# Kernel optimization log

Hardware: AMD Instinct MI355X
Metric: run time of the kernel (lower is better)

Reference implementation:

```python
import jax, jax.numpy as jnp
import numpy as np

N = 100000   # nodes
E = 625000   # edges
D = 128      # feature / embedding dim
C = 40       # num classes
BN_EPS = 1e-5
L2_EPS = 1e-12


def setup_inputs() -> dict:
    key = jax.random.key(0)
    ks = jax.random.split(key, 8)
    s = 1.0 / np.sqrt(D)
    return {
        "x": jax.random.normal(ks[0], (N, D), dtype=jnp.float32),
        "edge_index": jax.random.randint(ks[1], (2, E), 0, N, dtype=jnp.int64),
        "W1": jax.random.normal(ks[2], (D, D), dtype=jnp.float32) * s,
        "b1": jnp.zeros((D,), jnp.float32),
        "W2": jax.random.normal(ks[3], (D, D), dtype=jnp.float32) * s,
        "b2": jnp.zeros((D,), jnp.float32),
        "W3": jax.random.normal(ks[4], (D, D), dtype=jnp.float32) * s,
        "b3": jnp.zeros((D,), jnp.float32),
        "g1": jnp.ones((D,), jnp.float32), "be1": jnp.zeros((D,), jnp.float32),
        "g2": jnp.ones((D,), jnp.float32), "be2": jnp.zeros((D,), jnp.float32),
        "g3": jnp.ones((D,), jnp.float32), "be3": jnp.zeros((D,), jnp.float32),
        "Wout": jax.random.normal(ks[5], (D, C), dtype=jnp.float32) * s,
        "bout": jnp.zeros((C,), jnp.float32),
    }


def _gcn_norm(edge_index, n):
    # PyG GCNConv default: add self loops, symmetric normalization
    loop = jnp.arange(n)
    src = jnp.concatenate([edge_index[0], loop])
    dst = jnp.concatenate([edge_index[1], loop])
    deg = jax.ops.segment_sum(jnp.ones_like(src, dtype=jnp.float32), dst, num_segments=n)
    dinv = jnp.where(deg > 0, jax.lax.rsqrt(deg), 0.0)
    norm = dinv[src] * dinv[dst]  # [E+N]
    return src, dst, norm


def _gcn_conv(x, W, b, src, dst, norm, n):
    h = x @ W                                # [N, D]
    msg = h[src] * norm[:, None]             # gather, [E+N, D]
    out = jax.ops.segment_sum(msg, dst, num_segments=n)  # scatter-add
    return out + b


def _bn(x, g, b):
    mu = jnp.mean(x, axis=0)
    var = jnp.var(x, axis=0)
    return (x - mu) * jax.lax.rsqrt(var + BN_EPS) * g + b


def _l2norm(x):
    n = jnp.sqrt(jnp.sum(x * x, axis=1, keepdims=True))
    return x / jnp.maximum(n, L2_EPS)


def reference(x, edge_index, W1, b1, W2, b2, W3, b3,
              g1, be1, g2, be2, g3, be3, Wout, bout):
    n = x.shape[0]
    src, dst, norm = _gcn_norm(edge_index, n)

    h = jax.nn.relu(_bn(_gcn_conv(x, W1, b1, src, dst, norm, n), g1, be1))
    h = _l2norm(h)
    r = h
    h = jax.nn.relu(_bn(_gcn_conv(h, W2, b2, src, dst, norm, n), g2, be2))
    h = _l2norm(h + r)
    r = h
    h = jax.nn.relu(_bn(_gcn_conv(h, W3, b3, src, dst, norm, n), g3, be3))
    h = _l2norm(h + r)

    return h @ Wout + bout  # node classification logits [N, C]
```

## Files before the change

### kernel.cpp

```cpp
#include <hip/hip_runtime.h>
#include <math.h>

#define DD 128
#define COUT 40
#define BN_EPS 1e-5f
#define L2_EPS 1e-12f

typedef __attribute__((ext_vector_type(8))) short bf16x8;
typedef __attribute__((ext_vector_type(4))) float f32x4;

static __device__ inline unsigned short f2bf(float f) {
    unsigned int x = __float_as_uint(f);
    unsigned int r = (x + 0x7FFFu + ((x >> 16) & 1u)) >> 16;
    return (unsigned short)r;
}
static __device__ inline float bf2f(unsigned short u) {
    return __uint_as_float(((unsigned int)u) << 16);
}


__global__ void k_init(int* deg, int* fill, int n) {
    int i = blockIdx.x * blockDim.x + threadIdx.x;
    if (i < n) { deg[i] = 1; fill[i] = 0; }
}

__global__ void k_hist(const int* ei, int E, int* deg) {
    int i = blockIdx.x * blockDim.x + threadIdx.x;
    if (i < E) atomicAdd(&deg[ei[E + i]], 1);
}

__global__ void k_dinv(const int* deg, float* dinv, int n) {
    int i = blockIdx.x * blockDim.x + threadIdx.x;
    if (i < n) dinv[i] = rsqrtf((float)deg[i]);
}

__global__ void k_scan_a(const int* deg, int* row_ptr, int* bsum, int n) {
    __shared__ int s[256];
    int t = threadIdx.x;
    int idx = blockIdx.x * 256 + t;
    int v = (idx < n) ? deg[idx] : 0;
    s[t] = v; __syncthreads();
    for (int off = 1; off < 256; off <<= 1) {
        int x = (t >= off) ? s[t - off] : 0;
        __syncthreads(); s[t] += x; __syncthreads();
    }
    if (idx <= n) row_ptr[idx] = s[t] - v;
    if (t == 255) bsum[blockIdx.x] = s[255];
}

__global__ void k_scan_b(const int* bsum, int* boff, int nb) {
    __shared__ int s[512];
    int t = threadIdx.x;
    int v = (t < nb) ? bsum[t] : 0;
    s[t] = v; __syncthreads();
    for (int off = 1; off < 512; off <<= 1) {
        int x = (t >= off) ? s[t - off] : 0;
        __syncthreads(); s[t] += x; __syncthreads();
    }
    if (t < nb) boff[t] = s[t] - v;
}

__global__ void k_scan_c(int* row_ptr, const int* boff, int n1) {
    int idx = blockIdx.x * blockDim.x + threadIdx.x;
    if (idx < n1) row_ptr[idx] += boff[idx >> 8];
}

__global__ void k_fill(const int* ei, int E, int n, const int* row_ptr,
                       const float* dinv, int* fill, int2* epair) {
    int i = blockIdx.x * blockDim.x + threadIdx.x;
    int total = E + n;
    if (i >= total) return;
    int u, v;
    if (i < E) { u = ei[i]; v = ei[E + i]; }
    else { u = i - E; v = u; }
    int p = atomicAdd(&fill[v], 1);
    int pos = row_ptr[v] + p;
    int2 pr; pr.x = u; pr.y = __float_as_int(dinv[u]);
    epair[pos] = pr;
}

__global__ void k_wrepack_all(const float* __restrict__ W1, const float* __restrict__ W2,
                              const float* __restrict__ W3, const float* __restrict__ Wout,
                              unsigned short* __restrict__ wb,
                              unsigned short* __restrict__ wob,
                              float* __restrict__ stats) {
    int b = blockIdx.x;
    if (b < 24) {
        int wi = b >> 3;
        const float* W = (wi == 0) ? W1 : (wi == 1) ? W2 : W3;
        unsigned short* out = wb + wi * 16384;
        int idx = (b & 7) * 256 + threadIdx.x;
        int kc = idx >> 9;
        int cc = (idx >> 6) & 7;
        int lane = idx & 63;
        int n = cc * 16 + (lane & 15);
        int kb = kc * 32 + (lane >> 4) * 8;
        unsigned short tmp[8];
#pragma unroll
        for (int j = 0; j < 8; j++) tmp[j] = f2bf(W[(size_t)(kb + j) * DD + n]);
        *(uint4*)&out[(size_t)idx * 8] = *(const uint4*)tmp;
    } else if (b < 27) {
        int idx = (b - 24) * 256 + threadIdx.x;
        int kc = idx / 192;
        int rem = idx % 192;
        int cc = rem >> 6;
        int lane = rem & 63;
        int n = cc * 16 + (lane & 15);
        int kb = kc * 32 + (lane >> 4) * 8;
        unsigned short tmp[8];
#pragma unroll
        for (int j = 0; j < 8; j++)
            tmp[j] = (n < COUT) ? f2bf(Wout[(size_t)(kb + j) * COUT + n]) : 0;
        *(uint4*)&wob[(size_t)idx * 8] = *(const uint4*)tmp;
    } else {
        stats[threadIdx.x] = 0.f;
        stats[256 + threadIdx.x] = 0.f;
        stats[512 + threadIdx.x] = 0.f;
    }
}


__global__ __launch_bounds__(256) void k_gemm0(const float* __restrict__ A,
                                               const unsigned short* __restrict__ Wb,
                                               unsigned short* __restrict__ C, int nrows) {
    __shared__ __align__(16) unsigned short Ws[16384];
    const int tid = threadIdx.x;
    for (int i = tid; i < 2048; i += 256)
        ((uint4*)Ws)[i] = ((const uint4*)Wb)[i];
    __syncthreads();

    const int wv = tid >> 6;
    const int lane = tid & 63;
    const int R0 = blockIdx.x * 64 + wv * 16;
    if (R0 >= nrows) return;
    const int m = lane & 15, q = lane >> 4;
    int rr = R0 + m; if (rr >= nrows) rr = nrows - 1;
    const float* Ar = A + (size_t)rr * DD + q * 8;

    bf16x8 af[4];
#pragma unroll
    for (int kc = 0; kc < 4; kc++) {
        float4 lo = *(const float4*)(Ar + kc * 32);
        float4 hi = *(const float4*)(Ar + kc * 32 + 4);
        unsigned short t[8];
        t[0] = f2bf(lo.x); t[1] = f2bf(lo.y); t[2] = f2bf(lo.z); t[3] = f2bf(lo.w);
        t[4] = f2bf(hi.x); t[5] = f2bf(hi.y); t[6] = f2bf(hi.z); t[7] = f2bf(hi.w);
        af[kc] = *(const bf16x8*)t;
    }

    f32x4 acc[8];
#pragma unroll
    for (int cc = 0; cc < 8; cc++) acc[cc] = (f32x4){0.f, 0.f, 0.f, 0.f};
#pragma unroll
    for (int kc = 0; kc < 4; kc++)
#pragma unroll
        for (int cc = 0; cc < 8; cc++) {
            bf16x8 b = *(const bf16x8*)&Ws[(size_t)((kc * 8 + cc) * 64 + lane) * 8];
            acc[cc] = __builtin_amdgcn_mfma_f32_16x16x32_bf16(af[kc], b, acc[cc], 0, 0, 0);
        }

#pragma unroll
    for (int cc = 0; cc < 8; cc++)
#pragma unroll
        for (int i = 0; i < 4; i++) {
            int r = R0 + q * 4 + i;
            if (r < nrows) C[(size_t)r * DD + cc * 16 + m] = f2bf(acc[cc][i]);
        }
}

__global__ void k_agg(const unsigned short* __restrict__ lin, const int* __restrict__ row_ptr,
                      const int2* __restrict__ epair, const float* __restrict__ dinv,
                      const float* __restrict__ bias, unsigned short* __restrict__ outb, int n) {
    int lane = threadIdx.x;
    int half = lane >> 5;
    int li = lane & 31;
    int v = blockIdx.x * 8 + threadIdx.y * 2 + half;
    if (v >= n) return;
    int c = li * 4;
    int s = row_ptr[v], e = row_ptr[v + 1];
    float dv = dinv[v];
    float4 accA = *(const float4*)&bias[c];
    float4 accB = make_float4(0.f, 0.f, 0.f, 0.f);
    int j = s;
    for (; j + 1 < e; j += 2) {
        int2 p0 = epair[j], p1 = epair[j + 1];
        float w0 = dv * __int_as_float(p0.y);
        float w1 = dv * __int_as_float(p1.y);
        ushort4 t0 = *(const ushort4*)&lin[(size_t)p0.x * DD + c];
        ushort4 t1 = *(const ushort4*)&lin[(size_t)p1.x * DD + c];
        accA.x += w0 * bf2f(t0.x); accA.y += w0 * bf2f(t0.y);
        accA.z += w0 * bf2f(t0.z); accA.w += w0 * bf2f(t0.w);
        accB.x += w1 * bf2f(t1.x); accB.y += w1 * bf2f(t1.y);
        accB.z += w1 * bf2f(t1.z); accB.w += w1 * bf2f(t1.w);
    }
    if (j < e) {
        int2 p = epair[j];
        float w = dv * __int_as_float(p.y);
        ushort4 t = *(const ushort4*)&lin[(size_t)p.x * DD + c];
        accA.x += w * bf2f(t.x); accA.y += w * bf2f(t.y);
        accA.z += w * bf2f(t.z); accA.w += w * bf2f(t.w);
    }
    accA.x += accB.x; accA.y += accB.y; accA.z += accB.z; accA.w += accB.w;
    ushort4 o;
    o.x = f2bf(accA.x); o.y = f2bf(accA.y); o.z = f2bf(accA.z); o.w = f2bf(accA.w);
    *(ushort4*)&outb[(size_t)v * DD + c] = o;
}

__global__ __launch_bounds__(256) void k_bnstats(const unsigned short* __restrict__ X, int n,
                                                 float* __restrict__ stats) {
    int cg = (threadIdx.x & 31) * 4;
    int rg = threadIdx.x >> 5;
    float s0 = 0, s1 = 0, s2 = 0, s3 = 0;
    float q0 = 0, q1 = 0, q2 = 0, q3 = 0;
    for (int r = blockIdx.x * 8 + rg; r < n; r += gridDim.x * 8) {
        ushort4 xv = *(const ushort4*)&X[(size_t)r * DD + cg];
        float x0 = bf2f(xv.x), x1 = bf2f(xv.y), x2 = bf2f(xv.z), x3 = bf2f(xv.w);
        s0 += x0; s1 += x1; s2 += x2; s3 += x3;
        q0 += x0 * x0; q1 += x1 * x1; q2 += x2 * x2; q3 += x3 * x3;
    }
    __shared__ float sh[8][128];
    __shared__ float qh[8][128];
    sh[rg][cg] = s0; sh[rg][cg + 1] = s1; sh[rg][cg + 2] = s2; sh[rg][cg + 3] = s3;
    qh[rg][cg] = q0; qh[rg][cg + 1] = q1; qh[rg][cg + 2] = q2; qh[rg][cg + 3] = q3;
    __syncthreads();
    if (threadIdx.x < 128) {
        float a = 0, b = 0;
        for (int g = 0; g < 8; g++) { a += sh[g][threadIdx.x]; b += qh[g][threadIdx.x]; }
        atomicAdd(&stats[threadIdx.x], a);
        atomicAdd(&stats[128 + threadIdx.x], b);
    }
}

template <bool HAS_RES>
__global__ __launch_bounds__(256) void k_fused(const unsigned short* __restrict__ aggX,
                                               const float* __restrict__ stats,
                                               const float* __restrict__ g,
                                               const float* __restrict__ be, float inv_n,
                                               const unsigned short* __restrict__ resb,
                                               const unsigned short* __restrict__ Wb,
                                               unsigned short* __restrict__ hbf_out,
                                               unsigned short* __restrict__ linb_out,
                                               int nrows) {
    __shared__ __align__(16) unsigned short Ws[16384];
    __shared__ float ssl[256];
    const int tid = threadIdx.x;
    for (int i = tid; i < 2048; i += 256)
        ((uint4*)Ws)[i] = ((const uint4*)Wb)[i];
    if (tid < 128) {
        float mu = stats[tid] * inv_n;
        float var = stats[128 + tid] * inv_n - mu * mu;
        float sc = g[tid] * rsqrtf(var + BN_EPS);
        ssl[tid] = sc;
        ssl[128 + tid] = be[tid] - mu * sc;
    }
    __syncthreads();

    const int wv = tid >> 6;
    const int lane = tid & 63;
    const int R0 = blockIdx.x * 64 + wv * 16;
    if (R0 >= nrows) return;
    const int m = lane & 15, q = lane >> 4;
    int rr = R0 + m; if (rr >= nrows) rr = nrows - 1;
    const unsigned short* Ar = aggX + (size_t)rr * DD + q * 8;
    const unsigned short* Rr = HAS_RES ? resb + (size_t)rr * DD + q * 8 : nullptr;

    float y[4][8];
    float sq = 0.f;
#pragma unroll
    for (int kc = 0; kc < 4; kc++) {
        ushort4 lo = *(const ushort4*)(Ar + kc * 32);
        ushort4 hi = *(const ushort4*)(Ar + kc * 32 + 4);
        unsigned short av[8] = {lo.x, lo.y, lo.z, lo.w, hi.x, hi.y, hi.z, hi.w};
        int c0 = kc * 32 + q * 8;
        float4 sc0 = *(const float4*)&ssl[c0];
        float4 sc1 = *(const float4*)&ssl[c0 + 4];
        float4 sh0 = *(const float4*)&ssl[128 + c0];
        float4 sh1 = *(const float4*)&ssl[128 + c0 + 4];
        float scv[8] = {sc0.x, sc0.y, sc0.z, sc0.w, sc1.x, sc1.y, sc1.z, sc1.w};
        float shv[8] = {sh0.x, sh0.y, sh0.z, sh0.w, sh1.x, sh1.y, sh1.z, sh1.w};
        if (HAS_RES) {
            ushort4 rl = *(const ushort4*)(Rr + kc * 32);
            ushort4 rh = *(const ushort4*)(Rr + kc * 32 + 4);
            unsigned short rv[8] = {rl.x, rl.y, rl.z, rl.w, rh.x, rh.y, rh.z, rh.w};
#pragma unroll
            for (int j = 0; j < 8; j++) {
                float yy = fmaxf(bf2f(av[j]) * scv[j] + shv[j], 0.f) + bf2f(rv[j]);
                y[kc][j] = yy; sq += yy * yy;
            }
        } else {
#pragma unroll
            for (int j = 0; j < 8; j++) {
                float yy = fmaxf(bf2f(av[j]) * scv[j] + shv[j], 0.f);
                y[kc][j] = yy; sq += yy * yy;
            }
        }
    }
    sq += __shfl_xor(sq, 16, 64);
    sq += __shfl_xor(sq, 32, 64);
    float inv = 1.f / fmaxf(sqrtf(sq), L2_EPS);

    bf16x8 af[4];
#pragma unroll
    for (int kc = 0; kc < 4; kc++) {
        unsigned short t[8];
#pragma unroll
        for (int j = 0; j < 8; j++) t[j] = f2bf(y[kc][j] * inv);
        af[kc] = *(const bf16x8*)t;
        *(bf16x8*)&hbf_out[(size_t)rr * DD + q * 8 + kc * 32] = af[kc];
    }

    f32x4 acc[8];
#pragma unroll
    for (int cc = 0; cc < 8; cc++) acc[cc] = (f32x4){0.f, 0.f, 0.f, 0.f};
#pragma unroll
    for (int kc = 0; kc < 4; kc++)
#pragma unroll
        for (int cc = 0; cc < 8; cc++) {
            bf16x8 b = *(const bf16x8*)&Ws[(size_t)((kc * 8 + cc) * 64 + lane) * 8];
            acc[cc] = __builtin_amdgcn_mfma_f32_16x16x32_bf16(af[kc], b, acc[cc], 0, 0, 0);
        }

#pragma unroll
    for (int cc = 0; cc < 8; cc++)
#pragma unroll
        for (int i = 0; i < 4; i++) {
            int r = R0 + q * 4 + i;
            if (r < nrows) linb_out[(size_t)r * DD + cc * 16 + m] = f2bf(acc[cc][i]);
        }
}

__global__ __launch_bounds__(256) void k_outfused(const unsigned short* __restrict__ aggX,
                                                  const float* __restrict__ stats,
                                                  const float* __restrict__ g,
                                                  const float* __restrict__ be, float inv_n,
                                                  const unsigned short* __restrict__ resb,
                                                  const unsigned short* __restrict__ wob,
                                                  const float* __restrict__ bout,
                                                  float* __restrict__ C, int nrows) {
    __shared__ __align__(16) unsigned short Ws[6144];
    __shared__ float ssl[256];
    const int tid = threadIdx.x;
    for (int i = tid; i < 768; i += 256)
        ((uint4*)Ws)[i] = ((const uint4*)wob)[i];
    if (tid < 128) {
        float mu = stats[tid] * inv_n;
        float var = stats[128 + tid] * inv_n - mu * mu;
        float sc = g[tid] * rsqrtf(var + BN_EPS);
        ssl[tid] = sc;
        ssl[128 + tid] = be[tid] - mu * sc;
    }
    __syncthreads();

    const int wv = tid >> 6;
    const int lane = tid & 63;
    const int R0 = blockIdx.x * 64 + wv * 16;
    if (R0 >= nrows) return;
    const int m = lane & 15, q = lane >> 4;
    int rr = R0 + m; if (rr >= nrows) rr = nrows - 1;
    const unsigned short* Ar = aggX + (size_t)rr * DD + q * 8;
    const unsigned short* Rr = resb + (size_t)rr * DD + q * 8;

    float y[4][8];
    float sq = 0.f;
#pragma unroll
    for (int kc = 0; kc < 4; kc++) {
        ushort4 lo = *(const ushort4*)(Ar + kc * 32);
        ushort4 hi = *(const ushort4*)(Ar + kc * 32 + 4);
        ushort4 rl = *(const ushort4*)(Rr + kc * 32);
        ushort4 rh = *(const ushort4*)(Rr + kc * 32 + 4);
        unsigned short av[8] = {lo.x, lo.y, lo.z, lo.w, hi.x, hi.y, hi.z, hi.w};
        unsigned short rv[8] = {rl.x, rl.y, rl.z, rl.w, rh.x, rh.y, rh.z, rh.w};
        int c0 = kc * 32 + q * 8;
        float4 sc0 = *(const float4*)&ssl[c0];
        float4 sc1 = *(const float4*)&ssl[c0 + 4];
        float4 sh0 = *(const float4*)&ssl[128 + c0];
        float4 sh1 = *(const float4*)&ssl[128 + c0 + 4];
        float scv[8] = {sc0.x, sc0.y, sc0.z, sc0.w, sc1.x, sc1.y, sc1.z, sc1.w};
        float shv[8] = {sh0.x, sh0.y, sh0.z, sh0.w, sh1.x, sh1.y, sh1.z, sh1.w};
#pragma unroll
        for (int j = 0; j < 8; j++) {
            float yy = fmaxf(bf2f(av[j]) * scv[j] + shv[j], 0.f) + bf2f(rv[j]);
            y[kc][j] = yy; sq += yy * yy;
        }
    }
    sq += __shfl_xor(sq, 16, 64);
    sq += __shfl_xor(sq, 32, 64);
    float inv = 1.f / fmaxf(sqrtf(sq), L2_EPS);

    bf16x8 af[4];
#pragma unroll
    for (int kc = 0; kc < 4; kc++) {
        unsigned short t[8];
#pragma unroll
        for (int j = 0; j < 8; j++) t[j] = f2bf(y[kc][j] * inv);
        af[kc] = *(const bf16x8*)t;
    }

    f32x4 acc[3];
#pragma unroll
    for (int cc = 0; cc < 3; cc++) acc[cc] = (f32x4){0.f, 0.f, 0.f, 0.f};
#pragma unroll
    for (int kc = 0; kc < 4; kc++)
#pragma unroll
        for (int cc = 0; cc < 3; cc++) {
            bf16x8 b = *(const bf16x8*)&Ws[(size_t)((kc * 3 + cc) * 64 + lane) * 8];
            acc[cc] = __builtin_amdgcn_mfma_f32_16x16x32_bf16(af[kc], b, acc[cc], 0, 0, 0);
        }

#pragma unroll
    for (int cc = 0; cc < 3; cc++) {
        int col = cc * 16 + m;
        if (col < COUT) {
            float bb = bout[col];
#pragma unroll
            for (int i = 0; i < 4; i++) {
                int r = R0 + q * 4 + i;
                if (r < nrows) C[(size_t)r * COUT + col] = acc[cc][i] + bb;
            }
        }
    }
}


extern "C" void kernel_launch(void* const* d_in, const int* in_sizes, int n_in,
                              void* d_out, int out_size, void* d_ws, size_t ws_size,
                              hipStream_t stream) {
    const float* x    = (const float*)d_in[0];
    const int*   ei   = (const int*)d_in[1];
    const float* W1   = (const float*)d_in[2];
    const float* b1   = (const float*)d_in[3];
    const float* W2   = (const float*)d_in[4];
    const float* b2   = (const float*)d_in[5];
    const float* W3   = (const float*)d_in[6];
    const float* b3   = (const float*)d_in[7];
    const float* g1   = (const float*)d_in[8];
    const float* be1  = (const float*)d_in[9];
    const float* g2   = (const float*)d_in[10];
    const float* be2  = (const float*)d_in[11];
    const float* g3   = (const float*)d_in[12];
    const float* be3  = (const float*)d_in[13];
    const float* Wout = (const float*)d_in[14];
    const float* bout = (const float*)d_in[15];
    float* out = (float*)d_out;

    const int N = in_sizes[0] / DD;
    const int E = in_sizes[1] / 2;
    const int NNZ = E + N;

    char* w = (char*)d_ws;
    unsigned short* linb = (unsigned short*)w; w += (size_t)N * DD * sizeof(unsigned short);
    unsigned short* aggA = (unsigned short*)w; w += (size_t)N * DD * sizeof(unsigned short);
    unsigned short* aggB = (unsigned short*)w; w += (size_t)N * DD * sizeof(unsigned short);
    unsigned short* hbf1 = (unsigned short*)w; w += (size_t)N * DD * sizeof(unsigned short);
    unsigned short* hbf2 = (unsigned short*)w; w += (size_t)N * DD * sizeof(unsigned short);
    unsigned short* wb   = (unsigned short*)w; w += 3 * 16384 * sizeof(unsigned short);
    unsigned short* wob  = (unsigned short*)w; w += 6144 * sizeof(unsigned short);
    int2* epair  = (int2*)w;                   w += (size_t)NNZ * sizeof(int2);
    int* deg     = (int*)w;                    w += (size_t)N * sizeof(int);
    int* fill    = (int*)w;                    w += (size_t)N * sizeof(int);
    int* row_ptr = (int*)w;                    w += (size_t)(N + 1) * sizeof(int);
    float* dinv  = (float*)w;                  w += (size_t)N * sizeof(float);
    int* bsum    = (int*)w;                    w += 512 * sizeof(int);
    int* boff    = (int*)w;                    w += 512 * sizeof(int);
    float* stats = (float*)w;                  w += 768 * sizeof(float);

    const int NB = (N + 1 + 255) / 256;
    const int STATS_GRID = 128;

    k_init<<<(N + 255) / 256, 256, 0, stream>>>(deg, fill, N);
    k_hist<<<(E + 255) / 256, 256, 0, stream>>>(ei, E, deg);
    k_dinv<<<(N + 255) / 256, 256, 0, stream>>>(deg, dinv, N);
    k_scan_a<<<NB, 256, 0, stream>>>(deg, row_ptr, bsum, N);
    k_scan_b<<<1, 512, 0, stream>>>(bsum, boff, NB);
    k_scan_c<<<(N + 1 + 255) / 256, 256, 0, stream>>>(row_ptr, boff, N + 1);
    k_fill<<<(NNZ + 255) / 256, 256, 0, stream>>>(ei, E, N, row_ptr, dinv, fill, epair);
    k_wrepack_all<<<28, 256, 0, stream>>>(W1, W2, W3, Wout, wb, wob, stats);

    int gemmGrid = (N + 63) / 64;
    dim3 aggGrid((N + 7) / 8);
    dim3 aggBlk(64, 4);
    float inv_n = 1.0f / (float)N;

    k_gemm0<<<gemmGrid, 256, 0, stream>>>(x, wb, linb, N);
    k_agg<<<aggGrid, aggBlk, 0, stream>>>(linb, row_ptr, epair, dinv, b1, aggA, N);
    k_bnstats<<<STATS_GRID, 256, 0, stream>>>(aggA, N, stats);
    k_fused<false><<<gemmGrid, 256, 0, stream>>>(aggA, stats, g1, be1, inv_n,
                                                 nullptr, wb + 16384, hbf1, linb, N);
    k_agg<<<aggGrid, aggBlk, 0, stream>>>(linb, row_ptr, epair, dinv, b2, aggB, N);
    k_bnstats<<<STATS_GRID, 256, 0, stream>>>(aggB, N, stats + 256);
    k_fused<true><<<gemmGrid, 256, 0, stream>>>(aggB, stats + 256, g2, be2, inv_n,
                                                hbf1, wb + 32768, hbf2, linb, N);
    k_agg<<<aggGrid, aggBlk, 0, stream>>>(linb, row_ptr, epair, dinv, b3, aggA, N);
    k_bnstats<<<STATS_GRID, 256, 0, stream>>>(aggA, N, stats + 512);
    k_outfused<<<gemmGrid, 256, 0, stream>>>(aggA, stats + 512, g3, be3, inv_n,
                                             hbf2, wob, bout, out, N);
}
```

Baseline: 474.1 us.

## Fuse BN statistics into aggregation and simplify CSR build with recorded atomic positions

Aggregation is rewritten so one wavefront handles one node. Four lane groups each take a different edge and load 8 bf16 channels, then combine partial sums with cross-lane shuffles. The same kernel accumulates the BatchNorm sum and sum of squares, which removes the separate stats pass that reread the aggregated features. CSR construction records each edge's atomic slot during the histogram, folds the dinv computation into the scan, places self-loops at the end of each row, and replaces the init kernel with a memset. Together these cut four launches, the fill atomics and one full feature reread per layer. The cost is a persistent grid of 2048 blocks that does more shuffle work, and the order of edges inside each row changes.

```diff
diff --git a/kernel.cpp b/kernel.cpp
--- a/kernel.cpp
+++ b/kernel.cpp
@@ -19,26 +19,19 @@
 }
 
 
-__global__ void k_init(int* deg, int* fill, int n) {
+__global__ void k_hist(const int* __restrict__ ei, int E, int* __restrict__ deg,
+                       int* __restrict__ pord) {
     int i = blockIdx.x * blockDim.x + threadIdx.x;
-    if (i < n) { deg[i] = 1; fill[i] = 0; }
-}
-
-__global__ void k_hist(const int* ei, int E, int* deg) {
-    int i = blockIdx.x * blockDim.x + threadIdx.x;
-    if (i < E) atomicAdd(&deg[ei[E + i]], 1);
-}
-
-__global__ void k_dinv(const int* deg, float* dinv, int n) {
-    int i = blockIdx.x * blockDim.x + threadIdx.x;
-    if (i < n) dinv[i] = rsqrtf((float)deg[i]);
-}
-
-__global__ void k_scan_a(const int* deg, int* row_ptr, int* bsum, int n) {
+    if (i < E) pord[i] = atomicAdd(&deg[ei[E + i]], 1);
+}
+
+__global__ void k_scan_a(const int* __restrict__ deg, int* __restrict__ row_ptr,
+                         int* __restrict__ bsum, float* __restrict__ dinv, int n) {
     __shared__ int s[256];
     int t = threadIdx.x;
     int idx = blockIdx.x * 256 + t;
-    int v = (idx < n) ? deg[idx] : 0;
+    int v = (idx < n) ? deg[idx] + 1 : 0;
+    if (idx < n) dinv[idx] = rsqrtf((float)v);
     s[t] = v; __syncthreads();
     for (int off = 1; off < 256; off <<= 1) {
         int x = (t >= off) ? s[t - off] : 0;
@@ -48,7 +41,7 @@
     if (t == 255) bsum[blockIdx.x] = s[255];
 }
 
-__global__ void k_scan_b(const int* bsum, int* boff, int nb) {
+__global__ void k_scan_b(const int* __restrict__ bsum, int* __restrict__ boff, int nb) {
     __shared__ int s[512];
     int t = threadIdx.x;
     int v = (t < nb) ? bsum[t] : 0;
@@ -60,21 +53,26 @@
     if (t < nb) boff[t] = s[t] - v;
 }
 
-__global__ void k_scan_c(int* row_ptr, const int* boff, int n1) {
+__global__ void k_scan_c(int* __restrict__ row_ptr, const int* __restrict__ boff, int n1) {
     int idx = blockIdx.x * blockDim.x + threadIdx.x;
     if (idx < n1) row_ptr[idx] += boff[idx >> 8];
 }
 
-__global__ void k_fill(const int* ei, int E, int n, const int* row_ptr,
-                       const float* dinv, int* fill, int2* epair) {
+__global__ void k_fill(const int* __restrict__ ei, const int* __restrict__ pord,
+                       int E, int n, const int* __restrict__ row_ptr,
+                       const float* __restrict__ dinv, int2* __restrict__ epair) {
     int i = blockIdx.x * blockDim.x + threadIdx.x;
     int total = E + n;
     if (i >= total) return;
-    int u, v;
-    if (i < E) { u = ei[i]; v = ei[E + i]; }
-    else { u = i - E; v = u; }
-    int p = atomicAdd(&fill[v], 1);
-    int pos = row_ptr[v] + p;
+    int u, pos;
+    if (i < E) {
+        u = ei[i];
+        int v = ei[E + i];
+        pos = row_ptr[v] + pord[i];
+    } else {
+        u = i - E;
+        pos = row_ptr[u + 1] - 1;
+    }
     int2 pr; pr.x = u; pr.y = __float_as_int(dinv[u]);
     epair[pos] = pr;
 }
@@ -168,66 +166,102 @@
         }
 }
 
-__global__ void k_agg(const unsigned short* __restrict__ lin, const int* __restrict__ row_ptr,
-                      const int2* __restrict__ epair, const float* __restrict__ dinv,
-                      const float* __restrict__ bias, unsigned short* __restrict__ outb, int n) {
-    int lane = threadIdx.x;
-    int half = lane >> 5;
-    int li = lane & 31;
-    int v = blockIdx.x * 8 + threadIdx.y * 2 + half;
-    if (v >= n) return;
-    int c = li * 4;
-    int s = row_ptr[v], e = row_ptr[v + 1];
-    float dv = dinv[v];
-    float4 accA = *(const float4*)&bias[c];
-    float4 accB = make_float4(0.f, 0.f, 0.f, 0.f);
-    int j = s;
-    for (; j + 1 < e; j += 2) {
-        int2 p0 = epair[j], p1 = epair[j + 1];
-        float w0 = dv * __int_as_float(p0.y);
-        float w1 = dv * __int_as_float(p1.y);
-        ushort4 t0 = *(const ushort4*)&lin[(size_t)p0.x * DD + c];
-        ushort4 t1 = *(const ushort4*)&lin[(size_t)p1.x * DD + c];
-        accA.x += w0 * bf2f(t0.x); accA.y += w0 * bf2f(t0.y);
-        accA.z += w0 * bf2f(t0.z); accA.w += w0 * bf2f(t0.w);
-        accB.x += w1 * bf2f(t1.x); accB.y += w1 * bf2f(t1.y);
-        accB.z += w1 * bf2f(t1.z); accB.w += w1 * bf2f(t1.w);
-    }
-    if (j < e) {
-        int2 p = epair[j];
-        float w = dv * __int_as_float(p.y);
-        ushort4 t = *(const ushort4*)&lin[(size_t)p.x * DD + c];
-        accA.x += w * bf2f(t.x); accA.y += w * bf2f(t.y);
-        accA.z += w * bf2f(t.z); accA.w += w * bf2f(t.w);
-    }
-    accA.x += accB.x; accA.y += accB.y; accA.z += accB.z; accA.w += accB.w;
-    ushort4 o;
-    o.x = f2bf(accA.x); o.y = f2bf(accA.y); o.z = f2bf(accA.z); o.w = f2bf(accA.w);
-    *(ushort4*)&outb[(size_t)v * DD + c] = o;
-}
-
-__global__ __launch_bounds__(256) void k_bnstats(const unsigned short* __restrict__ X, int n,
-                                                 float* __restrict__ stats) {
-    int cg = (threadIdx.x & 31) * 4;
-    int rg = threadIdx.x >> 5;
-    float s0 = 0, s1 = 0, s2 = 0, s3 = 0;
-    float q0 = 0, q1 = 0, q2 = 0, q3 = 0;
-    for (int r = blockIdx.x * 8 + rg; r < n; r += gridDim.x * 8) {
-        ushort4 xv = *(const ushort4*)&X[(size_t)r * DD + cg];
-        float x0 = bf2f(xv.x), x1 = bf2f(xv.y), x2 = bf2f(xv.z), x3 = bf2f(xv.w);
-        s0 += x0; s1 += x1; s2 += x2; s3 += x3;
-        q0 += x0 * x0; q1 += x1 * x1; q2 += x2 * x2; q3 += x3 * x3;
-    }
-    __shared__ float sh[8][128];
-    __shared__ float qh[8][128];
-    sh[rg][cg] = s0; sh[rg][cg + 1] = s1; sh[rg][cg + 2] = s2; sh[rg][cg + 3] = s3;
-    qh[rg][cg] = q0; qh[rg][cg + 1] = q1; qh[rg][cg + 2] = q2; qh[rg][cg + 3] = q3;
+__global__ __launch_bounds__(256) void k_aggs(const unsigned short* __restrict__ lin,
+                                              const int* __restrict__ row_ptr,
+                                              const int2* __restrict__ epair,
+                                              const float* __restrict__ dinv,
+                                              const float* __restrict__ bias,
+                                              unsigned short* __restrict__ outb,
+                                              float* __restrict__ stats, int n) {
+    const int tid = threadIdx.x;
+    const int wv = tid >> 6;
+    const int lane = tid & 63;
+    const int g = lane >> 4;
+    const int ci = (lane & 15) * 8;
+
+    float bs[8];
+    {
+        float4 b0 = *(const float4*)&bias[ci];
+        float4 b1 = *(const float4*)&bias[ci + 4];
+        bs[0] = b0.x; bs[1] = b0.y; bs[2] = b0.z; bs[3] = b0.w;
+        bs[4] = b1.x; bs[5] = b1.y; bs[6] = b1.z; bs[7] = b1.w;
+    }
+
+    float s[8], q[8];
+#pragma unroll
+    for (int k = 0; k < 8; k++) { s[k] = 0.f; q[k] = 0.f; }
+
+    const int wstride = gridDim.x * 4;
+    for (int v = blockIdx.x * 4 + wv; v < n; v += wstride) {
+        int rp0 = row_ptr[v];
+        int deg = row_ptr[v + 1] - rp0;
+        float dv = dinv[v];
+        float acc[8];
+#pragma unroll
+        for (int k = 0; k < 8; k++) acc[k] = 0.f;
+
+        for (int j = 0; j < deg; j += 8) {
+            int i0 = j + g;
+            int i1 = j + 4 + g;
+            if (i0 < deg) {
+                int2 p = epair[rp0 + i0];
+                float w = dv * __int_as_float(p.y);
+                uint4 t = *(const uint4*)&lin[(size_t)p.x * DD + ci];
+                acc[0] += w * __uint_as_float(t.x << 16);
+                acc[1] += w * __uint_as_float(t.x & 0xFFFF0000u);
+                acc[2] += w * __uint_as_float(t.y << 16);
+                acc[3] += w * __uint_as_float(t.y & 0xFFFF0000u);
+                acc[4] += w * __uint_as_float(t.z << 16);
+                acc[5] += w * __uint_as_float(t.z & 0xFFFF0000u);
+                acc[6] += w * __uint_as_float(t.w << 16);
+                acc[7] += w * __uint_as_float(t.w & 0xFFFF0000u);
+            }
+            if (i1 < deg) {
+                int2 p = epair[rp0 + i1];
+                float w = dv * __int_as_float(p.y);
+                uint4 t = *(const uint4*)&lin[(size_t)p.x * DD + ci];
+                acc[0] += w * __uint_as_float(t.x << 16);
+                acc[1] += w * __uint_as_float(t.x & 0xFFFF0000u);
+                acc[2] += w * __uint_as_float(t.y << 16);
+                acc[3] += w * __uint_as_float(t.y & 0xFFFF0000u);
+                acc[4] += w * __uint_as_float(t.z << 16);
+                acc[5] += w * __uint_as_float(t.z & 0xFFFF0000u);
+                acc[6] += w * __uint_as_float(t.w << 16);
+                acc[7] += w * __uint_as_float(t.w & 0xFFFF0000u);
+            }
+        }
+
+#pragma unroll
+        for (int k = 0; k < 8; k++) {
+            acc[k] += __shfl_xor(acc[k], 16, 64);
+            acc[k] += __shfl_xor(acc[k], 32, 64);
+            acc[k] += bs[k];
+        }
+
+        if (g == 0) {
+            unsigned short t[8];
+#pragma unroll
+            for (int k = 0; k < 8; k++) {
+                t[k] = f2bf(acc[k]);
+                s[k] += acc[k];
+                q[k] += acc[k] * acc[k];
+            }
+            *(uint4*)&outb[(size_t)v * DD + ci] = *(const uint4*)t;
+        }
+    }
+
+    __shared__ float sh[4][128];
+    __shared__ float qh[4][128];
+    if (g == 0) {
+#pragma unroll
+        for (int k = 0; k < 8; k++) { sh[wv][ci + k] = s[k]; qh[wv][ci + k] = q[k]; }
+    }
     __syncthreads();
-    if (threadIdx.x < 128) {
-        float a = 0, b = 0;
-        for (int g = 0; g < 8; g++) { a += sh[g][threadIdx.x]; b += qh[g][threadIdx.x]; }
-        atomicAdd(&stats[threadIdx.x], a);
-        atomicAdd(&stats[128 + threadIdx.x], b);
+    if (tid < 128) {
+        float a = sh[0][tid] + sh[1][tid] + sh[2][tid] + sh[3][tid];
+        float b = qh[0][tid] + qh[1][tid] + qh[2][tid] + qh[3][tid];
+        atomicAdd(&stats[tid], a);
+        atomicAdd(&stats[128 + tid], b);
     }
 }
 
@@ -456,8 +490,8 @@
     unsigned short* wb   = (unsigned short*)w; w += 3 * 16384 * sizeof(unsigned short);
     unsigned short* wob  = (unsigned short*)w; w += 6144 * sizeof(unsigned short);
     int2* epair  = (int2*)w;                   w += (size_t)NNZ * sizeof(int2);
+    int* pord    = (int*)w;                    w += (size_t)E * sizeof(int);
     int* deg     = (int*)w;                    w += (size_t)N * sizeof(int);
-    int* fill    = (int*)w;                    w += (size_t)N * sizeof(int);
     int* row_ptr = (int*)w;                    w += (size_t)(N + 1) * sizeof(int);
     float* dinv  = (float*)w;                  w += (size_t)N * sizeof(float);
     int* bsum    = (int*)w;                    w += 512 * sizeof(int);
@@ -465,33 +499,27 @@
     float* stats = (float*)w;                  w += 768 * sizeof(float);
 
     const int NB = (N + 1 + 255) / 256;
-    const int STATS_GRID = 128;
-
-    k_init<<<(N + 255) / 256, 256, 0, stream>>>(deg, fill, N);
-    k_hist<<<(E + 255) / 256, 256, 0, stream>>>(ei, E, deg);
-    k_dinv<<<(N + 255) / 256, 256, 0, stream>>>(deg, dinv, N);
-    k_scan_a<<<NB, 256, 0, stream>>>(deg, row_ptr, bsum, N);
+
+    hipMemsetAsync(deg, 0, (size_t)N * sizeof(int), stream);
+    k_wrepack_all<<<28, 256, 0, stream>>>(W1, W2, W3, Wout, wb, wob, stats);
+    k_hist<<<(E + 255) / 256, 256, 0, stream>>>(ei, E, deg, pord);
+    k_scan_a<<<NB, 256, 0, stream>>>(deg, row_ptr, bsum, dinv, N);
     k_scan_b<<<1, 512, 0, stream>>>(bsum, boff, NB);
     k_scan_c<<<(N + 1 + 255) / 256, 256, 0, stream>>>(row_ptr, boff, N + 1);
-    k_fill<<<(NNZ + 255) / 256, 256, 0, stream>>>(ei, E, N, row_ptr, dinv, fill, epair);
-    k_wrepack_all<<<28, 256, 0, stream>>>(W1, W2, W3, Wout, wb, wob, stats);
+    k_fill<<<(NNZ + 255) / 256, 256, 0, stream>>>(ei, pord, E, N, row_ptr, dinv, epair);
 
     int gemmGrid = (N + 63) / 64;
-    dim3 aggGrid((N + 7) / 8);
-    dim3 aggBlk(64, 4);
+    int aggGrid = 2048;
     float inv_n = 1.0f / (float)N;
 
     k_gemm0<<<gemmGrid, 256, 0, stream>>>(x, wb, linb, N);
-    k_agg<<<aggGrid, aggBlk, 0, stream>>>(linb, row_ptr, epair, dinv, b1, aggA, N);
-    k_bnstats<<<STATS_GRID, 256, 0, stream>>>(aggA, N, stats);
+    k_aggs<<<aggGrid, 256, 0, stream>>>(linb, row_ptr, epair, dinv, b1, aggA, stats, N);
     k_fused<false><<<gemmGrid, 256, 0, stream>>>(aggA, stats, g1, be1, inv_n,
                                                  nullptr, wb + 16384, hbf1, linb, N);
-    k_agg<<<aggGrid, aggBlk, 0, stream>>>(linb, row_ptr, epair, dinv, b2, aggB, N);
-    k_bnstats<<<STATS_GRID, 256, 0, stream>>>(aggB, N, stats + 256);
+    k_aggs<<<aggGrid, 256, 0, stream>>>(linb, row_ptr, epair, dinv, b2, aggB, stats + 256, N);
     k_fused<true><<<gemmGrid, 256, 0, stream>>>(aggB, stats + 256, g2, be2, inv_n,
                                                 hbf1, wb + 32768, hbf2, linb, N);
-    k_agg<<<aggGrid, aggBlk, 0, stream>>>(linb, row_ptr, epair, dinv, b3, aggA, N);
-    k_bnstats<<<STATS_GRID, 256, 0, stream>>>(aggA, N, stats + 512);
+    k_aggs<<<aggGrid, 256, 0, stream>>>(linb, row_ptr, epair, dinv, b3, aggA, stats + 512, N);
     k_outfused<<<gemmGrid, 256, 0, stream>>>(aggA, stats + 512, g3, be3, inv_n,
                                              hbf2, wob, bout, out, N);
 }
```

Measured after the change: 542.8 us. 14.5% more time.
